# Kernel tuning notes

Hardware: AMD Instinct MI355X
Metric: run time of the kernel (lower is better)

The kernel has to match this reference:

```python
import jax, jax.numpy as jnp
import numpy as np

B, CTX, QST, E, H = 8, 4096, 512, 300, 128

def setup_inputs() -> dict:
    key = jax.random.key(0)
    k1, k2, k3, k4 = jax.random.split(key, 4)
    context_sequence = jax.random.normal(k1, (B, CTX, E), dtype=jnp.float32)
    question_sequence = jax.random.normal(k2, (B, QST, E), dtype=jnp.float32)
    question_mask = jnp.ones((B, QST), dtype=jnp.int32)
    # dense layer params (PyTorch Linear: y = x @ W.T + b)
    bound = 1.0 / np.sqrt(E)
    W = jax.random.uniform(k3, (H, E), minval=-bound, maxval=bound, dtype=jnp.float32)
    b = jax.random.uniform(k4, (H,), minval=-bound, maxval=bound, dtype=jnp.float32)
    return {"context_sequence": context_sequence, "question_sequence": question_sequence,
            "question_mask": question_mask, "W": W, "b": b}

def reference(context_sequence, question_sequence, question_mask, W, b):
    # ReLU(dense(x)) for both sequences
    ctx_logits = jax.nn.relu(jnp.einsum('bce,he->bch', context_sequence, W) + b)   # [B, CTX, H]
    qst_logits = jax.nn.relu(jnp.einsum('bqe,he->bqh', question_sequence, W) + b)  # [B, QST, H]
    scores = jnp.einsum('bch,bqh->bcq', ctx_logits, qst_logits)                    # [B, CTX, QST]
    scores = jnp.where(question_mask[:, None, :] == 0, -jnp.inf, scores)
    attn = jax.nn.softmax(scores, axis=-1)
    return jnp.einsum('bcq,bqh->bch', attn, qst_logits)                            # [B, CTX, H]
```

## Files before the change

kernel.cpp:

```cpp
#include <hip/hip_runtime.h>
#include <hip/hip_bf16.h>

#define BB   8
#define SCTX 4096
#define SQ   512
#define EE   300
#define HH   128
#define EP   320
#define CST  328
#define LOG2E 1.4426950408889634f

typedef short bhalf4 __attribute__((ext_vector_type(4)));
typedef short short8 __attribute__((ext_vector_type(8)));
typedef float f32x4  __attribute__((ext_vector_type(4)));
typedef unsigned u32x4 __attribute__((ext_vector_type(4)));

#define MFMA16(a, b, c) __builtin_amdgcn_mfma_f32_16x16x32_bf16((a), (b), (c), 0, 0, 0)

__device__ __forceinline__ short f2bf(float f) {
  unsigned u = __builtin_bit_cast(unsigned, f);
  u += 0x7fffu + ((u >> 16) & 1u);
  return (short)(u >> 16);
}
__device__ __forceinline__ float bf2f(short s) {
  return __builtin_bit_cast(float, ((unsigned)(unsigned short)s) << 16);
}
__device__ __forceinline__ unsigned pack2(float a, float b) {
  return (unsigned)(unsigned short)f2bf(a) | ((unsigned)(unsigned short)f2bf(b) << 16);
}
__device__ __forceinline__ void gload16(const void* g, void* lds) {
  __builtin_amdgcn_global_load_lds(
      (const __attribute__((address_space(1))) void*)g,
      (__attribute__((address_space(3))) void*)lds, 16, 0, 0);
}

__global__ void k_wpad(const float* __restrict__ W, short* __restrict__ wsw) {
  const int h = blockIdx.x, k = threadIdx.x;
  float v = (k < EE) ? W[h * EE + k] : 0.0f;
  const int m = h >> 4, t = h & 15, kk = k >> 5, quad = (k >> 3) & 3, j = k & 7;
  wsw[((kk * 8 + m) * 64 + quad * 16 + t) * 8 + j] = f2bf(v);
}

__global__ __launch_bounds__(256) void k_qlog(const float* __restrict__ qst,
                                              const short* __restrict__ wsw,
                                              const float* __restrict__ bias,
                                              short* __restrict__ ql,
                                              short* __restrict__ qlT) {
  const int b = blockIdx.y;
  const int m0 = blockIdx.x * 32;
  const int tid = threadIdx.x;
  const int w = tid >> 6, l = tid & 63, t = l & 15, quad = l >> 4;
  const int g = w >> 1, hf = w & 1;

  __shared__ __align__(16) short cst[32 * CST];

  const float4* cbase = (const float4*)(qst + (size_t)(b * SQ + m0) * EE);
#pragma unroll
  for (int j = 0; j < 10; ++j) {
    int i4 = tid + j * 256;
    if (i4 < 2400) {
      float4 v = cbase[i4];
      int row = i4 / 75, c4 = i4 - row * 75;
      short* dp = cst + row * CST + c4 * 4;
      dp[0] = f2bf(v.x); dp[1] = f2bf(v.y); dp[2] = f2bf(v.z); dp[3] = f2bf(v.w);
    }
  }
  for (int i = tid; i < 320; i += 256) {
    int row = i / 10, c = (i - row * 10) * 2;
    cst[row * CST + 300 + c] = 0;
    cst[row * CST + 301 + c] = 0;
  }
  __syncthreads();

  const short* arow = cst + (g * 16 + t) * CST;
  f32x4 acc[4] = {};
#pragma unroll
  for (int kk = 0; kk < 10; ++kk) {
    const int k = kk * 32 + quad * 8;
    short8 a = *(const short8*)(arow + k);
#pragma unroll
    for (int n = 0; n < 4; ++n) {
      short8 w8 = *(const short8*)(wsw + ((kk * 8 + hf * 4 + n) * 64 + l) * 8);
      acc[n] = MFMA16(a, w8, acc[n]);
    }
  }
#pragma unroll
  for (int n = 0; n < 4; ++n) {
    const int h = (hf * 4 + n) * 16 + t;
    const float bv = bias[h];
#pragma unroll
    for (int r = 0; r < 4; ++r) {
      float v = fmaxf(acc[n][r] + bv, 0.0f);
      short s16 = f2bf(v);
      const int row = m0 + g * 16 + quad * 4 + r;
      ql[((size_t)b * SQ + row) * HH + h] = s16;
      qlT[((size_t)b * HH + h) * SQ + row] = s16;
    }
  }
}

__global__ __launch_bounds__(256, 2) void k_attn(const float* __restrict__ ctx,
                                                 const short* __restrict__ wsw,
                                                 const float* __restrict__ bias,
                                                 const int* __restrict__ mask,
                                                 const short* __restrict__ ql,
                                                 const short* __restrict__ qlT,
                                                 float* __restrict__ out) {
  const int b = blockIdx.y;
  const int m0 = blockIdx.x * 64;
  const int tid = threadIdx.x;
  const int w = tid >> 6, l = tid & 63, t = l & 15, quad = l >> 4;
  const int g = w >> 1, hf = w & 1;

  __shared__ __align__(16) short uq[16384];
  __shared__ __align__(16) short uv[16384];
  __shared__ short maskh[SQ];
  short* cst = uq;
  short* qch = uq;
  short* clt = uv;
  short* vch = uv;

  for (int i = tid; i < SQ; i += 256)
    maskh[i] = f2bf(mask[b * SQ + i] ? -8.0f : -1e30f);

  for (int i = 0; i < 2; ++i) {
    const float4* cbase = (const float4*)(ctx + ((size_t)b * SCTX + m0 + i * 32) * EE);
#pragma unroll
    for (int j = 0; j < 10; ++j) {
      int i4 = tid + j * 256;
      if (i4 < 2400) {
        float4 v = cbase[i4];
        int row = i4 / 75, c4 = i4 - row * 75;
        short* dp = cst + row * CST + c4 * 4;
        dp[0] = f2bf(v.x); dp[1] = f2bf(v.y); dp[2] = f2bf(v.z); dp[3] = f2bf(v.w);
      }
    }
    for (int k = tid; k < 320; k += 256) {
      int row = k / 10, c = (k - row * 10) * 2;
      cst[row * CST + 300 + c] = 0;
      cst[row * CST + 301 + c] = 0;
    }
    __syncthreads();
    const short* arow = cst + (g * 16 + t) * CST;
    f32x4 acc[4] = {};
#pragma unroll
    for (int kk = 0; kk < 10; ++kk) {
      const int k = kk * 32 + quad * 8;
      short8 a = *(const short8*)(arow + k);
#pragma unroll
      for (int n = 0; n < 4; ++n) {
        short8 w8 = *(const short8*)(wsw + ((kk * 8 + hf * 4 + n) * 64 + l) * 8);
        acc[n] = MFMA16(a, w8, acc[n]);
      }
    }
#pragma unroll
    for (int n = 0; n < 4; ++n) {
      const int h = (hf * 4 + n) * 16 + t;
      const float bv = bias[h];
#pragma unroll
      for (int r = 0; r < 4; ++r) {
        float v = fmaxf(acc[n][r] + bv, 0.0f);
        clt[(i * 32 + g * 16 + quad * 4 + r) * 136 + h] = f2bf(v);
      }
    }
    __syncthreads();
  }

  short8 af[4];
#pragma unroll
  for (int kk = 0; kk < 4; ++kk)
    af[kk] = *(const short8*)&clt[(w * 16 + t) * 136 + kk * 32 + quad * 8];
  __syncthreads();

  const int srcA = ((quad & 1) * 2) * 16 + t;
  const int srcB = srcA + 16;
  const bool hiq = quad >= 2;
  const int sx = (t & 7) << 3;
  const int rl = l >> 4;
  const int cb = (l & 15) * 16;

  f32x4 o[8] = {};
  float rtot = 0.0f;
  for (int c = 0; c < 4; ++c) {
#pragma unroll
    for (int s = 0; s < 8; ++s) {
      const int row = w * 32 + s * 4 + rl;
      const int sw = cb ^ ((row & 7) << 4);
      gload16((const char*)(ql + ((size_t)b * SQ + c * 128 + row) * HH) + sw,
              qch + (w * 32 + s * 4) * 128);
      gload16((const char*)(qlT + ((size_t)b * HH + row) * SQ + c * 128) + sw,
              vch + (w * 32 + s * 4) * 128);
    }
    __syncthreads();

#pragma unroll
    for (int kk = 0; kk < 4; ++kk) {
      f32x4 svE = {0.f, 0.f, 0.f, 0.f}, svO = {0.f, 0.f, 0.f, 0.f};
      const short* qrE = qch + ((kk * 2) * 16 + t) * 128;
      const short* qrO = qrE + 16 * 128;
#pragma unroll
      for (int kx = 0; kx < 4; ++kx) {
        const int co = (kx * 32 + quad * 8) ^ sx;
        short8 b8e = *(const short8*)(qrE + co);
        short8 b8o = *(const short8*)(qrO + co);
        svE = MFMA16(b8e, af[kx], svE);
        svO = MFMA16(b8o, af[kx], svO);
      }
      bhalf4 mbE = *(const bhalf4*)&maskh[c * 128 + (kk * 2) * 16 + quad * 4];
      bhalf4 mbO = *(const bhalf4*)&maskh[c * 128 + (kk * 2 + 1) * 16 + quad * 4];
      float pE[4], pO[4];
#pragma unroll
      for (int r = 0; r < 4; ++r) {
        pE[r] = exp2f((svE[r] + bf2f(mbE[r])) * LOG2E);
        pO[r] = exp2f((svO[r] + bf2f(mbO[r])) * LOG2E);
        rtot += pE[r] + pO[r];
      }
      unsigned pkE0 = pack2(pE[0], pE[1]), pkE1 = pack2(pE[2], pE[3]);
      unsigned pkO0 = pack2(pO[0], pO[1]), pkO1 = pack2(pO[2], pO[3]);
      unsigned sE0 = (unsigned)__shfl((int)pkE0, srcA), sE1 = (unsigned)__shfl((int)pkE1, srcA);
      unsigned sO0 = (unsigned)__shfl((int)pkO0, srcA), sO1 = (unsigned)__shfl((int)pkO1, srcA);
      unsigned tE0 = (unsigned)__shfl((int)pkE0, srcB), tE1 = (unsigned)__shfl((int)pkE1, srcB);
      unsigned tO0 = (unsigned)__shfl((int)pkO0, srcB), tO1 = (unsigned)__shfl((int)pkO1, srcB);
      u32x4 av;
      av[0] = hiq ? sO0 : sE0;
      av[1] = hiq ? sO1 : sE1;
      av[2] = hiq ? tO0 : tE0;
      av[3] = hiq ? tO1 : tE1;
      short8 pa = __builtin_bit_cast(short8, av);
#pragma unroll
      for (int n = 0; n < 8; ++n) {
        const int co = (kk * 32 + quad * 8) ^ sx;
        short8 v8 = *(const short8*)&vch[(n * 16 + t) * 128 + co];
        o[n] = MFMA16(pa, v8, o[n]);
      }
    }
    __syncthreads();
  }

  rtot += __shfl_xor(rtot, 16);
  rtot += __shfl_xor(rtot, 32);
  f32x4 rinv;
#pragma unroll
  for (int r = 0; r < 4; ++r) rinv[r] = 1.0f / __shfl(rtot, quad * 4 + r);
  float* obase = out + ((size_t)b * SCTX + m0 + w * 16) * HH;
#pragma unroll
  for (int n = 0; n < 8; ++n)
#pragma unroll
    for (int r = 0; r < 4; ++r)
      obase[(quad * 4 + r) * HH + n * 16 + t] = o[n][r] * rinv[r];
}

extern "C" void kernel_launch(void* const* d_in, const int* in_sizes, int n_in,
                              void* d_out, int out_size, void* d_ws, size_t ws_size,
                              hipStream_t stream) {
  const float* ctx  = (const float*)d_in[0];
  const float* qst  = (const float*)d_in[1];
  const int*   mask = (const int*)d_in[2];
  const float* W    = (const float*)d_in[3];
  const float* bias = (const float*)d_in[4];
  float* out = (float*)d_out;

  short* wsw  = (short*)d_ws;
  short* ql   = (short*)((char*)d_ws + 81920);
  short* qlT  = ql + (size_t)BB * SQ * HH;

  k_wpad<<<dim3(HH), dim3(EP), 0, stream>>>(W, wsw);
  k_qlog<<<dim3(SQ / 32, BB), dim3(256), 0, stream>>>(qst, wsw, bias, ql, qlT);
  k_attn<<<dim3(SCTX / 64, BB), dim3(256), 0, stream>>>(ctx, wsw, bias, mask, ql, qlT, out);
}
```

Before: 122.0 us.

## Split Q/V staging to overlap chunk loads with score and PV compute

The attention loop now stages Q and V chunks separately. V for the current chunk loads while QK scores are computed. The next Q chunk loads while the PV MFMAs run, and one barrier is dropped. Smaller changes vectorize the bf16 LDS stores and the transposed qlT global stores, and batch weight-fragment loads ahead of the MFMAs. The costs are more live registers (score arrays, shuffled packs) and a more delicate barrier ordering around the shared LDS buffers.

```diff
diff --git a/kernel.cpp b/kernel.cpp
--- a/kernel.cpp
+++ b/kernel.cpp
@@ -61,14 +61,13 @@
     if (i4 < 2400) {
       float4 v = cbase[i4];
       int row = i4 / 75, c4 = i4 - row * 75;
-      short* dp = cst + row * CST + c4 * 4;
-      dp[0] = f2bf(v.x); dp[1] = f2bf(v.y); dp[2] = f2bf(v.z); dp[3] = f2bf(v.w);
+      bhalf4 s4; s4[0] = f2bf(v.x); s4[1] = f2bf(v.y); s4[2] = f2bf(v.z); s4[3] = f2bf(v.w);
+      *(bhalf4*)(cst + row * CST + c4 * 4) = s4;
     }
   }
   for (int i = tid; i < 320; i += 256) {
     int row = i / 10, c = (i - row * 10) * 2;
-    cst[row * CST + 300 + c] = 0;
-    cst[row * CST + 301 + c] = 0;
+    *(int*)&cst[row * CST + 300 + c] = 0;
   }
   __syncthreads();
 
@@ -78,24 +77,27 @@
   for (int kk = 0; kk < 10; ++kk) {
     const int k = kk * 32 + quad * 8;
     short8 a = *(const short8*)(arow + k);
-#pragma unroll
-    for (int n = 0; n < 4; ++n) {
-      short8 w8 = *(const short8*)(wsw + ((kk * 8 + hf * 4 + n) * 64 + l) * 8);
-      acc[n] = MFMA16(a, w8, acc[n]);
-    }
+    short8 w8[4];
+#pragma unroll
+    for (int n = 0; n < 4; ++n)
+      w8[n] = *(const short8*)(wsw + ((kk * 8 + hf * 4 + n) * 64 + l) * 8);
+#pragma unroll
+    for (int n = 0; n < 4; ++n) acc[n] = MFMA16(a, w8[n], acc[n]);
   }
 #pragma unroll
   for (int n = 0; n < 4; ++n) {
     const int h = (hf * 4 + n) * 16 + t;
     const float bv = bias[h];
+    bhalf4 s4;
 #pragma unroll
     for (int r = 0; r < 4; ++r) {
       float v = fmaxf(acc[n][r] + bv, 0.0f);
       short s16 = f2bf(v);
+      s4[r] = s16;
       const int row = m0 + g * 16 + quad * 4 + r;
       ql[((size_t)b * SQ + row) * HH + h] = s16;
-      qlT[((size_t)b * HH + h) * SQ + row] = s16;
-    }
+    }
+    *(bhalf4*)&qlT[((size_t)b * HH + h) * SQ + m0 + g * 16 + quad * 4] = s4;
   }
 }
 
@@ -131,14 +133,13 @@
       if (i4 < 2400) {
         float4 v = cbase[i4];
         int row = i4 / 75, c4 = i4 - row * 75;
-        short* dp = cst + row * CST + c4 * 4;
-        dp[0] = f2bf(v.x); dp[1] = f2bf(v.y); dp[2] = f2bf(v.z); dp[3] = f2bf(v.w);
+        bhalf4 s4; s4[0] = f2bf(v.x); s4[1] = f2bf(v.y); s4[2] = f2bf(v.z); s4[3] = f2bf(v.w);
+        *(bhalf4*)(cst + row * CST + c4 * 4) = s4;
       }
     }
     for (int k = tid; k < 320; k += 256) {
       int row = k / 10, c = (k - row * 10) * 2;
-      cst[row * CST + 300 + c] = 0;
-      cst[row * CST + 301 + c] = 0;
+      *(int*)&cst[row * CST + 300 + c] = 0;
     }
     __syncthreads();
     const short* arow = cst + (g * 16 + t) * CST;
@@ -147,11 +148,12 @@
     for (int kk = 0; kk < 10; ++kk) {
       const int k = kk * 32 + quad * 8;
       short8 a = *(const short8*)(arow + k);
-#pragma unroll
-      for (int n = 0; n < 4; ++n) {
-        short8 w8 = *(const short8*)(wsw + ((kk * 8 + hf * 4 + n) * 64 + l) * 8);
-        acc[n] = MFMA16(a, w8, acc[n]);
-      }
+      short8 w8[4];
+#pragma unroll
+      for (int n = 0; n < 4; ++n)
+        w8[n] = *(const short8*)(wsw + ((kk * 8 + hf * 4 + n) * 64 + l) * 8);
+#pragma unroll
+      for (int n = 0; n < 4; ++n) acc[n] = MFMA16(a, w8[n], acc[n]);
     }
 #pragma unroll
     for (int n = 0; n < 4; ++n) {
@@ -170,7 +172,6 @@
 #pragma unroll
   for (int kk = 0; kk < 4; ++kk)
     af[kk] = *(const short8*)&clt[(w * 16 + t) * 136 + kk * 32 + quad * 8];
-  __syncthreads();
 
   const int srcA = ((quad & 1) * 2) * 16 + t;
   const int srcB = srcA + 16;
@@ -179,62 +180,88 @@
   const int rl = l >> 4;
   const int cb = (l & 15) * 16;
 
-  f32x4 o[8] = {};
-  float rtot = 0.0f;
-  for (int c = 0; c < 4; ++c) {
+  auto stageQ = [&](int c) {
 #pragma unroll
     for (int s = 0; s < 8; ++s) {
       const int row = w * 32 + s * 4 + rl;
       const int sw = cb ^ ((row & 7) << 4);
       gload16((const char*)(ql + ((size_t)b * SQ + c * 128 + row) * HH) + sw,
               qch + (w * 32 + s * 4) * 128);
+    }
+  };
+  auto stageV = [&](int c) {
+#pragma unroll
+    for (int s = 0; s < 8; ++s) {
+      const int row = w * 32 + s * 4 + rl;
+      const int sw = cb ^ ((row & 7) << 4);
       gload16((const char*)(qlT + ((size_t)b * HH + row) * SQ + c * 128) + sw,
               vch + (w * 32 + s * 4) * 128);
     }
-    __syncthreads();
-
+  };
+
+  stageQ(0);
+
+  f32x4 o[8] = {};
+  float rtot = 0.0f;
+  for (int c = 0; c < 4; ++c) {
+    __syncthreads();
+    stageV(c);
+
+    f32x4 sv[8] = {};
 #pragma unroll
     for (int kk = 0; kk < 4; ++kk) {
-      f32x4 svE = {0.f, 0.f, 0.f, 0.f}, svO = {0.f, 0.f, 0.f, 0.f};
       const short* qrE = qch + ((kk * 2) * 16 + t) * 128;
       const short* qrO = qrE + 16 * 128;
 #pragma unroll
       for (int kx = 0; kx < 4; ++kx) {
         const int co = (kx * 32 + quad * 8) ^ sx;
-        short8 b8e = *(const short8*)(qrE + co);
-        short8 b8o = *(const short8*)(qrO + co);
-        svE = MFMA16(b8e, af[kx], svE);
-        svO = MFMA16(b8o, af[kx], svO);
-      }
+        sv[kk * 2]     = MFMA16(*(const short8*)(qrE + co), af[kx], sv[kk * 2]);
+        sv[kk * 2 + 1] = MFMA16(*(const short8*)(qrO + co), af[kx], sv[kk * 2 + 1]);
+      }
+    }
+    unsigned pk[16];
+#pragma unroll
+    for (int kk = 0; kk < 4; ++kk) {
       bhalf4 mbE = *(const bhalf4*)&maskh[c * 128 + (kk * 2) * 16 + quad * 4];
       bhalf4 mbO = *(const bhalf4*)&maskh[c * 128 + (kk * 2 + 1) * 16 + quad * 4];
       float pE[4], pO[4];
 #pragma unroll
       for (int r = 0; r < 4; ++r) {
-        pE[r] = exp2f((svE[r] + bf2f(mbE[r])) * LOG2E);
-        pO[r] = exp2f((svO[r] + bf2f(mbO[r])) * LOG2E);
+        pE[r] = exp2f((sv[kk * 2][r] + bf2f(mbE[r])) * LOG2E);
+        pO[r] = exp2f((sv[kk * 2 + 1][r] + bf2f(mbO[r])) * LOG2E);
         rtot += pE[r] + pO[r];
       }
-      unsigned pkE0 = pack2(pE[0], pE[1]), pkE1 = pack2(pE[2], pE[3]);
-      unsigned pkO0 = pack2(pO[0], pO[1]), pkO1 = pack2(pO[2], pO[3]);
-      unsigned sE0 = (unsigned)__shfl((int)pkE0, srcA), sE1 = (unsigned)__shfl((int)pkE1, srcA);
-      unsigned sO0 = (unsigned)__shfl((int)pkO0, srcA), sO1 = (unsigned)__shfl((int)pkO1, srcA);
-      unsigned tE0 = (unsigned)__shfl((int)pkE0, srcB), tE1 = (unsigned)__shfl((int)pkE1, srcB);
-      unsigned tO0 = (unsigned)__shfl((int)pkO0, srcB), tO1 = (unsigned)__shfl((int)pkO1, srcB);
+      pk[kk * 4 + 0] = pack2(pE[0], pE[1]);
+      pk[kk * 4 + 1] = pack2(pE[2], pE[3]);
+      pk[kk * 4 + 2] = pack2(pO[0], pO[1]);
+      pk[kk * 4 + 3] = pack2(pO[2], pO[3]);
+    }
+    unsigned sA[16], sB[16];
+#pragma unroll
+    for (int i = 0; i < 16; ++i) {
+      sA[i] = (unsigned)__shfl((int)pk[i], srcA);
+      sB[i] = (unsigned)__shfl((int)pk[i], srcB);
+    }
+
+    __syncthreads();
+
+    if (c < 3) stageQ(c + 1);
+
+#pragma unroll
+    for (int kk = 0; kk < 4; ++kk) {
       u32x4 av;
-      av[0] = hiq ? sO0 : sE0;
-      av[1] = hiq ? sO1 : sE1;
-      av[2] = hiq ? tO0 : tE0;
-      av[3] = hiq ? tO1 : tE1;
+      av[0] = hiq ? sA[kk * 4 + 2] : sA[kk * 4 + 0];
+      av[1] = hiq ? sA[kk * 4 + 3] : sA[kk * 4 + 1];
+      av[2] = hiq ? sB[kk * 4 + 2] : sB[kk * 4 + 0];
+      av[3] = hiq ? sB[kk * 4 + 3] : sB[kk * 4 + 1];
       short8 pa = __builtin_bit_cast(short8, av);
+      const int co = (kk * 32 + quad * 8) ^ sx;
 #pragma unroll
       for (int n = 0; n < 8; ++n) {
-        const int co = (kk * 32 + quad * 8) ^ sx;
         short8 v8 = *(const short8*)&vch[(n * 16 + t) * 128 + co];
         o[n] = MFMA16(pa, v8, o[n]);
       }
     }
-    __syncthreads();
   }
 
   rtot += __shfl_xor(rtot, 16);
```

Measured after the change: 121.1 us. No clear change (-0.7%).
